# Kernel tuning notes

Hardware: AMD Instinct MI355X
Metric: run time of the kernel (lower is better)

Reference implementation:

```python
import jax, jax.numpy as jnp
import numpy as np
import math

N, E, O, C, KD, KEYD = 50000, 800000, 4, 64, 16, 128


def setup_inputs() -> dict:
    key = jax.random.key(0)
    ks = jax.random.split(key, 10)
    x = jax.random.normal(ks[0], (N, O, C), jnp.float32)
    kernel_basis = jax.random.normal(ks[1], (E, O, KD), jnp.float32)
    fiber_kernel_basis = jax.random.normal(ks[2], (O, O, KD), jnp.float32)
    edge_index = jax.random.randint(ks[3], (2, E), 0, N, jnp.int32)
    # nn.Linear default init ~ U(-1/sqrt(fan_in), 1/sqrt(fan_in)); scaled normal is fine as data
    kernel_W = jax.random.normal(ks[4], (C, KD), jnp.float32) / math.sqrt(KD)        # kernel: Linear(kernel_dim -> in_channels)
    fiber_kernel_W = jax.random.normal(ks[5], (C, KD), jnp.float32) / math.sqrt(KD)  # depthwise: in*out/groups = C
    key_W = jax.random.normal(ks[6], (KEYD, C), jnp.float32) / math.sqrt(C)
    key_b = jnp.zeros((KEYD,), jnp.float32)
    query_W = jax.random.normal(ks[7], (KEYD, C), jnp.float32) / math.sqrt(C)
    query_b = jnp.zeros((KEYD,), jnp.float32)
    bias = jnp.zeros((C,), jnp.float32)
    return {"x": x, "kernel_basis": kernel_basis, "fiber_kernel_basis": fiber_kernel_basis,
            "edge_index": edge_index, "kernel_W": kernel_W, "fiber_kernel_W": fiber_kernel_W,
            "key_W": key_W, "key_b": key_b, "query_W": query_W, "query_b": query_b, "bias": bias}


def reference(x, kernel_basis, fiber_kernel_basis, edge_index, kernel_W, fiber_kernel_W,
              key_W, key_b, query_W, query_b, bias):
    src = edge_index[0]
    dst = edge_index[1]
    n = x.shape[0]
    # per-edge spatial kernel: [E,O,KD] @ [KD,C] -> [E,O,C]
    k = jnp.einsum('eok,ck->eoc', kernel_basis, kernel_W)
    message = x[src] * k                                       # [E,O,C]
    # scatter-softmax attention over incoming edges of each target node
    keys = jnp.einsum('noc,kc->nok', x, key_W) + key_b        # [N,O,KEYD]
    queries = jnp.einsum('noc,kc->nok', x, query_W) + query_b
    logits = jnp.sum(keys[src] * queries[dst], axis=-1, keepdims=True) / math.sqrt(KEYD)  # [E,O,1]
    e = jnp.exp(logits - jnp.max(logits))                      # global-max stabilization, as in source
    denom = jax.ops.segment_sum(e, dst, num_segments=n) + 1e-6 # [N,O,1]
    att = e / denom[dst]
    message = message * att
    # scatter-add aggregation into target nodes
    x1 = jax.ops.segment_sum(message, dst, num_segments=n)     # [N,O,C]
    # fiber (orientation) mixing kernel: [O,O,KD] @ [KD,C] -> [O,O,C]
    fk = jnp.einsum('pok,ck->poc', fiber_kernel_basis, fiber_kernel_W)
    x2 = jnp.einsum('boc,poc->bpc', x1, fk) / fk.shape[-2]
    return x2 + bias
```

## Files before the change

### kernel.cpp

```cpp
#include <hip/hip_runtime.h>
#include <math.h>

#define NN 50000
#define EE 800000
#define OO 4
#define CC 64
#define KDD 16
#define KEYDD 128
#define CH 16

typedef float v2f __attribute__((ext_vector_type(2)));

__device__ __forceinline__ float wave_red_sum(float v) {
  int x;
  x = __builtin_amdgcn_update_dpp(0, __float_as_int(v), 0x111, 0xf, 0xf, false);
  v += __int_as_float(x);
  x = __builtin_amdgcn_update_dpp(0, __float_as_int(v), 0x112, 0xf, 0xf, false);
  v += __int_as_float(x);
  x = __builtin_amdgcn_update_dpp(0, __float_as_int(v), 0x114, 0xf, 0xf, false);
  v += __int_as_float(x);
  x = __builtin_amdgcn_update_dpp(0, __float_as_int(v), 0x118, 0xf, 0xf, false);
  v += __int_as_float(x);
  x = __builtin_amdgcn_update_dpp(0, __float_as_int(v), 0x142, 0xa, 0xf, false);
  v += __int_as_float(x);
  x = __builtin_amdgcn_update_dpp(0, __float_as_int(v), 0x143, 0xc, 0xf, false);
  v += __int_as_float(x);
  return __int_as_float(__builtin_amdgcn_readlane(__float_as_int(v), 63));
}

__device__ __forceinline__ float exp2_fast(float x) {
  float r;
  asm("v_exp_f32 %0, %1" : "=v"(r) : "v"(x));
  return r;
}

__device__ __forceinline__ void red4(float q0, float q1, float q2, float q3,
                                     float& p0, float& p1, float& p2, float& p3) {
  asm("s_nop 1\n\tv_permlane32_swap_b32 %0, %1" : "+v"(q0), "+v"(q1));
  float ra = q0 + q1;
  asm("s_nop 1\n\tv_permlane32_swap_b32 %0, %1" : "+v"(q2), "+v"(q3));
  float rb = q2 + q3;
  asm("s_nop 1\n\t"
      "v_add_f32_dpp %0, %0, %0 row_shr:1 row_mask:0xf bank_mask:0xf bound_ctrl:0\n\t"
      "v_add_f32_dpp %1, %1, %1 row_shr:1 row_mask:0xf bank_mask:0xf bound_ctrl:0\n\t"
      "v_add_f32_dpp %0, %0, %0 row_shr:2 row_mask:0xf bank_mask:0xf bound_ctrl:0\n\t"
      "v_add_f32_dpp %1, %1, %1 row_shr:2 row_mask:0xf bank_mask:0xf bound_ctrl:0\n\t"
      "v_add_f32_dpp %0, %0, %0 row_shr:4 row_mask:0xf bank_mask:0xf bound_ctrl:0\n\t"
      "v_add_f32_dpp %1, %1, %1 row_shr:4 row_mask:0xf bank_mask:0xf bound_ctrl:0\n\t"
      "v_add_f32_dpp %0, %0, %0 row_shr:8 row_mask:0xf bank_mask:0xf bound_ctrl:0\n\t"
      "v_add_f32_dpp %1, %1, %1 row_shr:8 row_mask:0xf bank_mask:0xf bound_ctrl:0\n\t"
      "v_add_f32_dpp %0, %0, %0 row_bcast:15 row_mask:0xa bank_mask:0xf bound_ctrl:0\n\t"
      "v_add_f32_dpp %1, %1, %1 row_bcast:15 row_mask:0xa bank_mask:0xf bound_ctrl:0\n\t"
      "s_nop 0"
      : "+v"(ra), "+v"(rb));
  p0 = __int_as_float(__builtin_amdgcn_readlane(__float_as_int(ra), 31));
  p1 = __int_as_float(__builtin_amdgcn_readlane(__float_as_int(ra), 63));
  p2 = __int_as_float(__builtin_amdgcn_readlane(__float_as_int(rb), 31));
  p3 = __int_as_float(__builtin_amdgcn_readlane(__float_as_int(rb), 63));
}

__global__ void prep_kernel(const float* __restrict__ keyW, const float* __restrict__ keyB,
                            const float* __restrict__ qryW, const float* __restrict__ qryB,
                            const float* __restrict__ fkb, const float* __restrict__ fkw,
                            float* __restrict__ Mt, float* __restrict__ aVec,
                            float* __restrict__ bVec, float* __restrict__ c0,
                            float* __restrict__ fk) {
  __shared__ float qw[KEYDD * CC];
  __shared__ float kws[KEYDD * 4];
  int t = threadIdx.x, b = blockIdx.x;
  if (b < 16) {
    for (int i = t; i < KEYDD * CC; i += 256) qw[i] = qryW[i];
    for (int i = t; i < KEYDD * 4; i += 256) {
      int k = i >> 2, c1l = i & 3;
      kws[i] = keyW[k * CC + b * 4 + c1l];
    }
    __syncthreads();
    int c1l = t >> 6, c2 = t & 63;
    float s = 0.f;
    #pragma unroll 8
    for (int k = 0; k < KEYDD; ++k)
      s = fmaf(kws[k * 4 + c1l], qw[k * CC + c2], s);
    Mt[c2 * CC + b * 4 + c1l] = s;
  } else {
    if (t < CC) {
      float sa = 0.f, sb = 0.f;
      for (int k = 0; k < KEYDD; ++k) {
        sa = fmaf(keyB[k], qryW[k * CC + t], sa);
        sb = fmaf(qryB[k], keyW[k * CC + t], sb);
      }
      aVec[t] = sa; bVec[t] = sb;
    }
    if (t == 0) {
      float s = 0.f;
      for (int k = 0; k < KEYDD; ++k) s = fmaf(keyB[k], qryB[k], s);
      c0[0] = s;
    }
    for (int idx = t; idx < OO * OO * CC; idx += 256) {
      int p = idx >> 8, rem = idx & 255;
      int o = rem >> 6, c = rem & 63;
      float s = 0.f;
      #pragma unroll
      for (int kd = 0; kd < KDD; ++kd)
        s = fmaf(fkb[(p * OO + o) * KDD + kd], fkw[c * KDD + kd], s);
      fk[idx] = 0.25f * s;
    }
  }
}

__global__ void count_kernel(const int* __restrict__ ei, int* __restrict__ counts) {
  int e = blockIdx.x * 256 + threadIdx.x;
  if (e < EE) atomicAdd(&counts[ei[EE + e]], 1);
}

__global__ void scan1_kernel(const int* __restrict__ counts, int* __restrict__ incl,
                             int* __restrict__ bsum, int n) {
  __shared__ int buf[256];
  int t = threadIdx.x;
  int i = blockIdx.x * 256 + t;
  int v = (i < n) ? counts[i] : 0;
  buf[t] = v;
  __syncthreads();
  for (int off = 1; off < 256; off <<= 1) {
    int a = buf[t];
    int b2 = (t >= off) ? buf[t - off] : 0;
    __syncthreads();
    buf[t] = a + b2;
    __syncthreads();
  }
  if (i < n) incl[i] = buf[t];
  if (t == 255) bsum[blockIdx.x] = buf[255];
}
__global__ void scan2_kernel(const int* __restrict__ bsum, int* __restrict__ bbase, int nb) {
  __shared__ int buf[256];
  int t = threadIdx.x;
  int v = (t < nb) ? bsum[t] : 0;
  buf[t] = v;
  __syncthreads();
  for (int off = 1; off < 256; off <<= 1) {
    int a = buf[t];
    int b2 = (t >= off) ? buf[t - off] : 0;
    __syncthreads();
    buf[t] = a + b2;
    __syncthreads();
  }
  if (t < nb) bbase[t] = buf[t] - v;
}
__global__ void scan3_kernel(const int* __restrict__ counts, const int* __restrict__ incl,
                             const int* __restrict__ bbase, int* __restrict__ offsets, int n) {
  int i = blockIdx.x * 256 + threadIdx.x;
  if (i < n) {
    int oi = bbase[blockIdx.x] + incl[i];
    offsets[i] = oi - counts[i];
    if (i == n - 1) offsets[n] = oi;
  }
}

__global__ void fill_kernel(const int* __restrict__ ei, const int* __restrict__ offsets,
                            int* __restrict__ counts, long long* __restrict__ pairs) {
  int e = blockIdx.x * 256 + threadIdx.x;
  if (e < EE) {
    int d = ei[EE + e];
    int r = atomicSub(&counts[d], 1) - 1;
    int pos = offsets[d] + r;
    pairs[pos] = ((long long)ei[e] << 32) | (unsigned)e;
  }
}

__device__ __forceinline__ float kv_dot(const float* __restrict__ kb, int ej, int obase,
                                        float4 kw0, float4 kw1, float4 kw2, float4 kw3) {
  const float4* bp = reinterpret_cast<const float4*>(kb + ej * (OO * KDD) + obase);
  float4 b0 = bp[0], b1 = bp[1], b2 = bp[2], b3 = bp[3];
  v2f a0 = {0.f, 0.f}, a1 = {0.f, 0.f};
  #define P2(f4, i) (reinterpret_cast<const v2f*>(&(f4))[i])
  a0 = __builtin_elementwise_fma(P2(b0, 0), P2(kw0, 0), a0);
  a1 = __builtin_elementwise_fma(P2(b0, 1), P2(kw0, 1), a1);
  a0 = __builtin_elementwise_fma(P2(b1, 0), P2(kw1, 0), a0);
  a1 = __builtin_elementwise_fma(P2(b1, 1), P2(kw1, 1), a1);
  a0 = __builtin_elementwise_fma(P2(b2, 0), P2(kw2, 0), a0);
  a1 = __builtin_elementwise_fma(P2(b2, 1), P2(kw2, 1), a1);
  a0 = __builtin_elementwise_fma(P2(b3, 0), P2(kw3, 0), a0);
  a1 = __builtin_elementwise_fma(P2(b3, 1), P2(kw3, 1), a1);
  #undef P2
  v2f s = a0 + a1;
  return s.x + s.y;
}

__global__ __launch_bounds__(256, 4) void mega_kernel(
    const float* __restrict__ x, const float* __restrict__ Mt,
    const float* __restrict__ aVec, const float* __restrict__ bVec,
    const float* __restrict__ c0p, const float* __restrict__ kb,
    const float* __restrict__ kW, const int* __restrict__ offsets,
    const long long* __restrict__ pairs, const float* __restrict__ fkg,
    const float* __restrict__ bias, float* __restrict__ out) {
  __shared__ float x1[OO * CC];
  int n = blockIdx.x;
  int t = threadIdx.x;
  int o = __builtin_amdgcn_readfirstlane(t >> 6);
  int c = t & 63;
  const float scale2 = 0.12751541050862828f;
  int js = offsets[n], je = offsets[n + 1];
  int deg = je - js;

  int lane16 = c & 15;
  long long pr = 0;
  if (deg > 0) pr = pairs[js + min(lane16, deg - 1)];

  int rowoff = __builtin_amdgcn_readfirstlane((n * OO + o) * CC);
  const float* xrow = x + rowoff;
  float ub0 = 0.f, ub1 = 0.f, ub2 = 0.f, ub3 = 0.f;
  #pragma unroll
  for (int q = 0; q < 16; ++q) {
    ub0 = fmaf(Mt[(4 * q + 0) * CC + c], xrow[4 * q + 0], ub0);
    ub1 = fmaf(Mt[(4 * q + 1) * CC + c], xrow[4 * q + 1], ub1);
    ub2 = fmaf(Mt[(4 * q + 2) * CC + c], xrow[4 * q + 2], ub2);
    ub3 = fmaf(Mt[(4 * q + 3) * CC + c], xrow[4 * q + 3], ub3);
  }
  float ubr = (((ub0 + ub1) + (ub2 + ub3)) + bVec[c]) * scale2;
  float xown = xrow[c];
  float base2 = (wave_red_sum(aVec[c] * xown) + c0p[0]) * scale2;

  const float4* kwp = reinterpret_cast<const float4*>(kW + c * KDD);
  float4 kw0 = kwp[0], kw1 = kwp[1], kw2 = kwp[2], kw3 = kwp[3];
  int obase = o * KDD;
  int voff = c << 2;

  float S = 0.f, acc = 0.f;

  for (int cs = 0; cs < deg; cs += CH) {
    int cl = deg - cs; if (cl > CH) cl = CH;
    int e_v = (int)((unsigned long long)pr & 0xffffffffu);
    int s_v = (int)(pr >> 32);
    float xv[CH];
    #pragma unroll
    for (int j = 0; j < CH; ++j) {
      int sj = __builtin_amdgcn_readlane(s_v, j);
      const float* pj = x + (size_t)(sj * OO + o) * CC;
      asm volatile("global_load_dword %0, %1, %2"
                   : "=v"(xv[j]) : "v"(voff), "s"(pj));
    }
    asm volatile("s_waitcnt vmcnt(0)" ::: "memory");
    __builtin_amdgcn_sched_barrier(0);
    int ns = cs + CH;
    if (ns < deg) {
      int ncl = deg - ns;
      pr = pairs[js + ns + min(lane16, ncl - 1)];
    }
    __builtin_amdgcn_sched_barrier(0);
    #define SUB4(J0)                                                           \
    {                                                                          \
      float kv0 = kv_dot(kb, __builtin_amdgcn_readlane(e_v, (J0) + 0), obase, kw0, kw1, kw2, kw3); \
      float kv1 = kv_dot(kb, __builtin_amdgcn_readlane(e_v, (J0) + 1), obase, kw0, kw1, kw2, kw3); \
      float kv2 = kv_dot(kb, __builtin_amdgcn_readlane(e_v, (J0) + 2), obase, kw0, kw1, kw2, kw3); \
      float kv3 = kv_dot(kb, __builtin_amdgcn_readlane(e_v, (J0) + 3), obase, kw0, kw1, kw2, kw3); \
      float p0, p1, p2, p3;                                                    \
      red4(xv[(J0) + 0] * ubr, xv[(J0) + 1] * ubr,                             \
           xv[(J0) + 2] * ubr, xv[(J0) + 3] * ubr, p0, p1, p2, p3);            \
      float ev0 = ((J0) + 0 < cl) ? exp2_fast(p0) : 0.f;                       \
      float ev1 = ((J0) + 1 < cl) ? exp2_fast(p1) : 0.f;                       \
      float ev2 = ((J0) + 2 < cl) ? exp2_fast(p2) : 0.f;                       \
      float ev3 = ((J0) + 3 < cl) ? exp2_fast(p3) : 0.f;                       \
      S += (ev0 + ev1) + (ev2 + ev3);                                          \
      acc = fmaf(ev0 * kv0, xv[(J0) + 0], acc);                                \
      acc = fmaf(ev1 * kv1, xv[(J0) + 1], acc);                                \
      acc = fmaf(ev2 * kv2, xv[(J0) + 2], acc);                                \
      acc = fmaf(ev3 * kv3, xv[(J0) + 3], acc);                                \
    }
    SUB4(0)
    if (cl > 4)  SUB4(4)
    if (cl > 8)  SUB4(8)
    if (cl > 12) SUB4(12)
    #undef SUB4
  }

  float invd = 1.0f / (S + 1e-6f * exp2_fast(-base2));
  x1[t] = acc * invd;
  __syncthreads();
  float s2s = 0.f;
  #pragma unroll
  for (int oo = 0; oo < OO; ++oo)
    s2s = fmaf(x1[oo * CC + c], fkg[o * (OO * CC) + oo * CC + c], s2s);
  out[(size_t)n * (OO * CC) + t] = s2s + bias[c];
}

extern "C" void kernel_launch(void* const* d_in, const int* in_sizes, int n_in,
                              void* d_out, int out_size, void* d_ws, size_t ws_size,
                              hipStream_t stream) {
  const float* x    = (const float*)d_in[0];
  const float* kb   = (const float*)d_in[1];
  const float* fkb  = (const float*)d_in[2];
  const int*   ei   = (const int*)d_in[3];
  const float* kW   = (const float*)d_in[4];
  const float* fkW  = (const float*)d_in[5];
  const float* keyW = (const float*)d_in[6];
  const float* keyB = (const float*)d_in[7];
  const float* qryW = (const float*)d_in[8];
  const float* qryB = (const float*)d_in[9];
  const float* bias = (const float*)d_in[10];
  float* out = (float*)d_out;

  const int NB = (NN + 255) / 256;

  float* wsf  = (float*)d_ws;
  float* Mt   = wsf;
  float* aVec = Mt + 4096;
  float* bVec = aVec + 64;
  float* c0   = bVec + 64;
  float* fk   = c0 + 64;
  long long* pairs = (long long*)(fk + 1024);
  int* counts    = (int*)(pairs + EE);
  int* offsets   = counts + NN;
  int* incl      = offsets + NN + 1;
  int* bsum      = incl + NN;
  int* bbase     = bsum + 256;

  hipMemsetAsync(counts, 0, (size_t)NN * sizeof(int), stream);

  prep_kernel<<<17, 256, 0, stream>>>(keyW, keyB, qryW, qryB, fkb, fkW, Mt, aVec, bVec, c0, fk);
  count_kernel<<<(EE + 255) / 256, 256, 0, stream>>>(ei, counts);
  scan1_kernel<<<NB, 256, 0, stream>>>(counts, incl, bsum, NN);
  scan2_kernel<<<1, 256, 0, stream>>>(bsum, bbase, NB);
  scan3_kernel<<<NB, 256, 0, stream>>>(counts, incl, bbase, offsets, NN);
  fill_kernel<<<(EE + 255) / 256, 256, 0, stream>>>(ei, offsets, counts, pairs);
  mega_kernel<<<NN, 256, 0, stream>>>(x, Mt, aVec, bVec, c0, kb, kW, offsets, pairs,
                                      fk, bias, out);
}
```

Baseline: 407.5 us.

## Double-buffer neighbor gathers and split edge pairs into separate index arrays

The mega kernel's edge loop now uses two register buffers, so the x gathers for the next 16-edge chunk and the index loads for the chunk after are issued before the current chunk is computed. This hides gather latency behind the kernel-basis dot products and exp work. The packed 64-bit (src, edge) pairs are split into two int arrays that are loaded with inline asm. The cost is extra VGPRs for a second 16-float buffer and the edge-id arrays, which may lower occupancy under the 256x4 launch bounds. Nodes average 16 edges, so many have only one chunk and get little overlap.

```diff
diff --git a/kernel.cpp b/kernel.cpp
--- a/kernel.cpp
+++ b/kernel.cpp
@@ -156,13 +156,15 @@
 }
 
 __global__ void fill_kernel(const int* __restrict__ ei, const int* __restrict__ offsets,
-                            int* __restrict__ counts, long long* __restrict__ pairs) {
+                            int* __restrict__ counts, int* __restrict__ edge_list,
+                            int* __restrict__ esrc) {
   int e = blockIdx.x * 256 + threadIdx.x;
   if (e < EE) {
     int d = ei[EE + e];
     int r = atomicSub(&counts[d], 1) - 1;
     int pos = offsets[d] + r;
-    pairs[pos] = ((long long)ei[e] << 32) | (unsigned)e;
+    edge_list[pos] = e;
+    esrc[pos] = ei[e];
   }
 }
 
@@ -190,8 +192,9 @@
     const float* __restrict__ aVec, const float* __restrict__ bVec,
     const float* __restrict__ c0p, const float* __restrict__ kb,
     const float* __restrict__ kW, const int* __restrict__ offsets,
-    const long long* __restrict__ pairs, const float* __restrict__ fkg,
-    const float* __restrict__ bias, float* __restrict__ out) {
+    const int* __restrict__ edge_list, const int* __restrict__ esrc,
+    const float* __restrict__ fkg, const float* __restrict__ bias,
+    float* __restrict__ out) {
   __shared__ float x1[OO * CC];
   int n = blockIdx.x;
   int t = threadIdx.x;
@@ -200,10 +203,14 @@
   const float scale2 = 0.12751541050862828f;
   int js = offsets[n], je = offsets[n + 1];
   int deg = je - js;
-
   int lane16 = c & 15;
-  long long pr = 0;
-  if (deg > 0) pr = pairs[js + min(lane16, deg - 1)];
+
+  int eA = 0, sA = 0, eB = 0, sB = 0;
+  if (deg > 0) {
+    int q0 = (js + min(lane16, deg - 1)) << 2;
+    asm volatile("global_load_dword %0, %1, %2" : "=v"(eA) : "v"(q0), "s"(edge_list));
+    asm volatile("global_load_dword %0, %1, %2" : "=v"(sA) : "v"(q0), "s"(esrc));
+  }
 
   int rowoff = __builtin_amdgcn_readfirstlane((n * OO + o) * CC);
   const float* xrow = x + rowoff;
@@ -225,52 +232,102 @@
   int voff = c << 2;
 
   float S = 0.f, acc = 0.f;
-
-  for (int cs = 0; cs < deg; cs += CH) {
-    int cl = deg - cs; if (cl > CH) cl = CH;
-    int e_v = (int)((unsigned long long)pr & 0xffffffffu);
-    int s_v = (int)(pr >> 32);
-    float xv[CH];
-    #pragma unroll
-    for (int j = 0; j < CH; ++j) {
-      int sj = __builtin_amdgcn_readlane(s_v, j);
-      const float* pj = x + (size_t)(sj * OO + o) * CC;
-      asm volatile("global_load_dword %0, %1, %2"
-                   : "=v"(xv[j]) : "v"(voff), "s"(pj));
-    }
+  float xvA[CH], xvB[CH];
+
+  #define GATHER(XV, SV)                                                       \
+  {                                                                            \
+    _Pragma("unroll")                                                          \
+    for (int j = 0; j < CH; ++j) {                                             \
+      int sj = __builtin_amdgcn_readlane(SV, j);                               \
+      const float* pj = x + (size_t)(sj * OO + o) * CC;                        \
+      asm volatile("global_load_dword %0, %1, %2"                              \
+                   : "=v"(XV[j]) : "v"(voff), "s"(pj));                        \
+    }                                                                          \
+  }
+  #define SUB4(XV, ES, J0, CL)                                                 \
+  {                                                                            \
+    float kv0 = kv_dot(kb, ES[(J0) + 0], obase, kw0, kw1, kw2, kw3);           \
+    float kv1 = kv_dot(kb, ES[(J0) + 1], obase, kw0, kw1, kw2, kw3);           \
+    float kv2 = kv_dot(kb, ES[(J0) + 2], obase, kw0, kw1, kw2, kw3);           \
+    float kv3 = kv_dot(kb, ES[(J0) + 3], obase, kw0, kw1, kw2, kw3);           \
+    float p0, p1, p2, p3;                                                      \
+    red4(XV[(J0) + 0] * ubr, XV[(J0) + 1] * ubr,                               \
+         XV[(J0) + 2] * ubr, XV[(J0) + 3] * ubr, p0, p1, p2, p3);              \
+    float ev0 = ((J0) + 0 < (CL)) ? exp2_fast(p0) : 0.f;                       \
+    float ev1 = ((J0) + 1 < (CL)) ? exp2_fast(p1) : 0.f;                       \
+    float ev2 = ((J0) + 2 < (CL)) ? exp2_fast(p2) : 0.f;                       \
+    float ev3 = ((J0) + 3 < (CL)) ? exp2_fast(p3) : 0.f;                       \
+    S += (ev0 + ev1) + (ev2 + ev3);                                            \
+    acc = fmaf(ev0 * kv0, XV[(J0) + 0], acc);                                  \
+    acc = fmaf(ev1 * kv1, XV[(J0) + 1], acc);                                  \
+    acc = fmaf(ev2 * kv2, XV[(J0) + 2], acc);                                  \
+    acc = fmaf(ev3 * kv3, XV[(J0) + 3], acc);                                  \
+  }
+  #define COMPUTE(XV, ES, CL)                                                  \
+    SUB4(XV, ES, 0, CL)                                                        \
+    if ((CL) > 4)  SUB4(XV, ES, 4, CL)                                         \
+    if ((CL) > 8)  SUB4(XV, ES, 8, CL)                                         \
+    if ((CL) > 12) SUB4(XV, ES, 12, CL)
+
+  if (deg > 0) {
     asm volatile("s_waitcnt vmcnt(0)" ::: "memory");
     __builtin_amdgcn_sched_barrier(0);
-    int ns = cs + CH;
-    if (ns < deg) {
-      int ncl = deg - ns;
-      pr = pairs[js + ns + min(lane16, ncl - 1)];
-    }
-    __builtin_amdgcn_sched_barrier(0);
-    #define SUB4(J0)                                                           \
-    {                                                                          \
-      float kv0 = kv_dot(kb, __builtin_amdgcn_readlane(e_v, (J0) + 0), obase, kw0, kw1, kw2, kw3); \
-      float kv1 = kv_dot(kb, __builtin_amdgcn_readlane(e_v, (J0) + 1), obase, kw0, kw1, kw2, kw3); \
-      float kv2 = kv_dot(kb, __builtin_amdgcn_readlane(e_v, (J0) + 2), obase, kw0, kw1, kw2, kw3); \
-      float kv3 = kv_dot(kb, __builtin_amdgcn_readlane(e_v, (J0) + 3), obase, kw0, kw1, kw2, kw3); \
-      float p0, p1, p2, p3;                                                    \
-      red4(xv[(J0) + 0] * ubr, xv[(J0) + 1] * ubr,                             \
-           xv[(J0) + 2] * ubr, xv[(J0) + 3] * ubr, p0, p1, p2, p3);            \
-      float ev0 = ((J0) + 0 < cl) ? exp2_fast(p0) : 0.f;                       \
-      float ev1 = ((J0) + 1 < cl) ? exp2_fast(p1) : 0.f;                       \
-      float ev2 = ((J0) + 2 < cl) ? exp2_fast(p2) : 0.f;                       \
-      float ev3 = ((J0) + 3 < cl) ? exp2_fast(p3) : 0.f;                       \
-      S += (ev0 + ev1) + (ev2 + ev3);                                          \
-      acc = fmaf(ev0 * kv0, xv[(J0) + 0], acc);                                \
-      acc = fmaf(ev1 * kv1, xv[(J0) + 1], acc);                                \
-      acc = fmaf(ev2 * kv2, xv[(J0) + 2], acc);                                \
-      acc = fmaf(ev3 * kv3, xv[(J0) + 3], acc);                                \
-    }
-    SUB4(0)
-    if (cl > 4)  SUB4(4)
-    if (cl > 8)  SUB4(8)
-    if (cl > 12) SUB4(12)
-    #undef SUB4
-  }
+    GATHER(xvA, sA)
+    if (CH < deg) {
+      int rem = deg - CH;
+      int q1 = (js + CH + min(lane16, rem - 1)) << 2;
+      asm volatile("global_load_dword %0, %1, %2" : "=v"(eB) : "v"(q1), "s"(edge_list));
+      asm volatile("global_load_dword %0, %1, %2" : "=v"(sB) : "v"(q1), "s"(esrc));
+    }
+    int cs = 0;
+    while (true) {
+      asm volatile("s_waitcnt vmcnt(0)" ::: "memory");
+      __builtin_amdgcn_sched_barrier(0);
+      int cl = deg - cs; if (cl > CH) cl = CH;
+      int esA[CH];
+      #pragma unroll
+      for (int j = 0; j < CH; ++j) esA[j] = __builtin_amdgcn_readlane(eA, j);
+      bool hasNext = (cs + CH) < deg;
+      if (hasNext) {
+        GATHER(xvB, sB)
+        int ns2 = cs + 2 * CH;
+        if (ns2 < deg) {
+          int rem2 = deg - ns2;
+          int q2 = (js + ns2 + min(lane16, rem2 - 1)) << 2;
+          asm volatile("global_load_dword %0, %1, %2" : "=v"(eA) : "v"(q2), "s"(edge_list));
+          asm volatile("global_load_dword %0, %1, %2" : "=v"(sA) : "v"(q2), "s"(esrc));
+        }
+      }
+      __builtin_amdgcn_sched_barrier(0);
+      COMPUTE(xvA, esA, cl)
+      if (!hasNext) break;
+      cs += CH;
+      asm volatile("s_waitcnt vmcnt(0)" ::: "memory");
+      __builtin_amdgcn_sched_barrier(0);
+      cl = deg - cs; if (cl > CH) cl = CH;
+      int esB[CH];
+      #pragma unroll
+      for (int j = 0; j < CH; ++j) esB[j] = __builtin_amdgcn_readlane(eB, j);
+      hasNext = (cs + CH) < deg;
+      if (hasNext) {
+        GATHER(xvA, sA)
+        int ns2 = cs + 2 * CH;
+        if (ns2 < deg) {
+          int rem2 = deg - ns2;
+          int q2 = (js + ns2 + min(lane16, rem2 - 1)) << 2;
+          asm volatile("global_load_dword %0, %1, %2" : "=v"(eB) : "v"(q2), "s"(edge_list));
+          asm volatile("global_load_dword %0, %1, %2" : "=v"(sB) : "v"(q2), "s"(esrc));
+        }
+      }
+      __builtin_amdgcn_sched_barrier(0);
+      COMPUTE(xvB, esB, cl)
+      if (!hasNext) break;
+      cs += CH;
+    }
+  }
+  #undef COMPUTE
+  #undef SUB4
+  #undef GATHER
 
   float invd = 1.0f / (S + 1e-6f * exp2_fast(-base2));
   x1[t] = acc * invd;
@@ -306,8 +363,9 @@
   float* bVec = aVec + 64;
   float* c0   = bVec + 64;
   float* fk   = c0 + 64;
-  long long* pairs = (long long*)(fk + 1024);
-  int* counts    = (int*)(pairs + EE);
+  int* edge_list = (int*)(fk + 1024);
+  int* esrc      = edge_list + EE;
+  int* counts    = esrc + EE;
   int* offsets   = counts + NN;
   int* incl      = offsets + NN + 1;
   int* bsum      = incl + NN;
@@ -320,7 +378,7 @@
   scan1_kernel<<<NB, 256, 0, stream>>>(counts, incl, bsum, NN);
   scan2_kernel<<<1, 256, 0, stream>>>(bsum, bbase, NB);
   scan3_kernel<<<NB, 256, 0, stream>>>(counts, incl, bbase, offsets, NN);
-  fill_kernel<<<(EE + 255) / 256, 256, 0, stream>>>(ei, offsets, counts, pairs);
-  mega_kernel<<<NN, 256, 0, stream>>>(x, Mt, aVec, bVec, c0, kb, kW, offsets, pairs,
-                                      fk, bias, out);
-}
+  fill_kernel<<<(EE + 255) / 256, 256, 0, stream>>>(ei, offsets, counts, edge_list, esrc);
+  mega_kernel<<<NN, 256, 0, stream>>>(x, Mt, aVec, bVec, c0, kb, kW, offsets,
+                                      edge_list, esrc, fk, bias, out);
+}
```

After: 1.581 ms. 3.88x slower.

## Double-buffer per-edge kernel basis rows in LDS via async global-to-LDS loads

Applied to the files above, without the earlier changes.

Per-edge kernel_basis rows for each 16-edge chunk are now staged cooperatively into a double-buffered LDS array with global_load_lds, and the pair indices are prefetched two chunks ahead. Each wave fetches its share of the 256-byte rows, and the dot products read from LDS instead of issuing scalar-addressed global float4 loads per edge. The aim is to overlap the next chunk's basis fetch with the current chunk's compute and to avoid redundant global reads across the four orientation waves. The cost is a block-wide __syncthreads per chunk and extra LDS use, which may lower occupancy.

```diff
diff --git a/kernel.cpp b/kernel.cpp
--- a/kernel.cpp
+++ b/kernel.cpp
@@ -59,6 +59,12 @@
   p3 = __int_as_float(__builtin_amdgcn_readlane(__float_as_int(rb), 63));
 }
 
+__device__ __forceinline__ void async_cp16(const float* gsrc, float* ldst) {
+  __builtin_amdgcn_global_load_lds(
+      (const __attribute__((address_space(1))) unsigned int*)gsrc,
+      (__attribute__((address_space(3))) unsigned int*)ldst, 16, 0, 0);
+}
+
 __global__ void prep_kernel(const float* __restrict__ keyW, const float* __restrict__ keyB,
                             const float* __restrict__ qryW, const float* __restrict__ qryB,
                             const float* __restrict__ fkb, const float* __restrict__ fkw,
@@ -166,9 +172,9 @@
   }
 }
 
-__device__ __forceinline__ float kv_dot(const float* __restrict__ kb, int ej, int obase,
-                                        float4 kw0, float4 kw1, float4 kw2, float4 kw3) {
-  const float4* bp = reinterpret_cast<const float4*>(kb + ej * (OO * KDD) + obase);
+__device__ __forceinline__ float kv_dot_lds(const float* row,
+                                            float4 kw0, float4 kw1, float4 kw2, float4 kw3) {
+  const float4* bp = reinterpret_cast<const float4*>(row);
   float4 b0 = bp[0], b1 = bp[1], b2 = bp[2], b3 = bp[3];
   v2f a0 = {0.f, 0.f}, a1 = {0.f, 0.f};
   #define P2(f4, i) (reinterpret_cast<const v2f*>(&(f4))[i])
@@ -192,6 +198,7 @@
     const float* __restrict__ kW, const int* __restrict__ offsets,
     const long long* __restrict__ pairs, const float* __restrict__ fkg,
     const float* __restrict__ bias, float* __restrict__ out) {
+  __shared__ float kbL[2][CH * 64];
   __shared__ float x1[OO * CC];
   int n = blockIdx.x;
   int t = threadIdx.x;
@@ -200,10 +207,10 @@
   const float scale2 = 0.12751541050862828f;
   int js = offsets[n], je = offsets[n + 1];
   int deg = je - js;
-
   int lane16 = c & 15;
-  long long pr = 0;
-  if (deg > 0) pr = pairs[js + min(lane16, deg - 1)];
+
+  long long prA = 0;
+  if (deg > 0) prA = pairs[js + min(lane16, deg - 1)];
 
   int rowoff = __builtin_amdgcn_readfirstlane((n * OO + o) * CC);
   const float* xrow = x + rowoff;
@@ -223,13 +230,34 @@
   float4 kw0 = kwp[0], kw1 = kwp[1], kw2 = kwp[2], kw3 = kwp[3];
   int obase = o * KDD;
   int voff = c << 2;
+  int w4 = o * 4;
+  int ksel = c >> 4;
+
+  #define STAGE(BUF, EV)                                                       \
+  {                                                                            \
+    int e0 = __builtin_amdgcn_readlane(EV, w4 + 0);                            \
+    int e1 = __builtin_amdgcn_readlane(EV, w4 + 1);                            \
+    int e2 = __builtin_amdgcn_readlane(EV, w4 + 2);                            \
+    int e3 = __builtin_amdgcn_readlane(EV, w4 + 3);                            \
+    int elo = (ksel & 1) ? e1 : e0;                                            \
+    int ehi = (ksel & 1) ? e3 : e2;                                            \
+    int es = (ksel & 2) ? ehi : elo;                                           \
+    async_cp16(kb + (size_t)es * 64 + (c & 15) * 4, &kbL[BUF][w4 * 64]);       \
+  }
 
   float S = 0.f, acc = 0.f;
+
+  if (deg > 0) {
+    int eA0 = (int)((unsigned long long)prA & 0xffffffffu);
+    STAGE(0, eA0)
+  }
+  long long prB = 0;
+  if (CH < deg) prB = pairs[js + CH + min(lane16, deg - CH - 1)];
 
   for (int cs = 0; cs < deg; cs += CH) {
     int cl = deg - cs; if (cl > CH) cl = CH;
-    int e_v = (int)((unsigned long long)pr & 0xffffffffu);
-    int s_v = (int)(pr >> 32);
+    int buf = (cs >> 4) & 1;
+    int s_v = (int)(prA >> 32);
     float xv[CH];
     #pragma unroll
     for (int j = 0; j < CH; ++j) {
@@ -240,18 +268,22 @@
     }
     asm volatile("s_waitcnt vmcnt(0)" ::: "memory");
     __builtin_amdgcn_sched_barrier(0);
-    int ns = cs + CH;
-    if (ns < deg) {
-      int ncl = deg - ns;
-      pr = pairs[js + ns + min(lane16, ncl - 1)];
-    }
+    __syncthreads();
+    bool hasNext = (cs + CH) < deg;
+    if (hasNext) {
+      int eN = (int)((unsigned long long)prB & 0xffffffffu);
+      STAGE(buf ^ 1, eN)
+    }
+    prA = prB;
+    int ns2 = cs + 2 * CH;
+    if (ns2 < deg) prB = pairs[js + ns2 + min(lane16, deg - ns2 - 1)];
     __builtin_amdgcn_sched_barrier(0);
     #define SUB4(J0)                                                           \
     {                                                                          \
-      float kv0 = kv_dot(kb, __builtin_amdgcn_readlane(e_v, (J0) + 0), obase, kw0, kw1, kw2, kw3); \
-      float kv1 = kv_dot(kb, __builtin_amdgcn_readlane(e_v, (J0) + 1), obase, kw0, kw1, kw2, kw3); \
-      float kv2 = kv_dot(kb, __builtin_amdgcn_readlane(e_v, (J0) + 2), obase, kw0, kw1, kw2, kw3); \
-      float kv3 = kv_dot(kb, __builtin_amdgcn_readlane(e_v, (J0) + 3), obase, kw0, kw1, kw2, kw3); \
+      float kv0 = kv_dot_lds(&kbL[buf][((J0) + 0) * 64 + obase], kw0, kw1, kw2, kw3); \
+      float kv1 = kv_dot_lds(&kbL[buf][((J0) + 1) * 64 + obase], kw0, kw1, kw2, kw3); \
+      float kv2 = kv_dot_lds(&kbL[buf][((J0) + 2) * 64 + obase], kw0, kw1, kw2, kw3); \
+      float kv3 = kv_dot_lds(&kbL[buf][((J0) + 3) * 64 + obase], kw0, kw1, kw2, kw3); \
       float p0, p1, p2, p3;                                                    \
       red4(xv[(J0) + 0] * ubr, xv[(J0) + 1] * ubr,                             \
            xv[(J0) + 2] * ubr, xv[(J0) + 3] * ubr, p0, p1, p2, p3);            \
@@ -271,6 +303,7 @@
     if (cl > 12) SUB4(12)
     #undef SUB4
   }
+  #undef STAGE
 
   float invd = 1.0f / (S + 1e-6f * exp2_fast(-base2));
   x1[t] = acc * invd;
```

Measured after the change: 436.4 us. +7.1%, slower.

## Double-buffer neighbor gathers with all edge pairs preloaded per wave

Applied to the files above, without the earlier changes.

Loads up to 64 (edge, src) pairs per node once into lanes instead of reloading 16 per chunk. The gather loop becomes a ping-pong double buffer of 8-element chunks, so the next chunk's x-row loads are issued before the current chunk is computed. This hides gather latency behind the dot-product and exp work. Nodes with degree above 64 fall back to a serial per-edge tail loop, which is slow but rare for average degree 16. The extra register buffer may raise register pressure.

```diff
diff --git a/kernel.cpp b/kernel.cpp
--- a/kernel.cpp
+++ b/kernel.cpp
@@ -7,7 +7,7 @@
 #define CC 64
 #define KDD 16
 #define KEYDD 128
-#define CH 16
+#define CH 8
 
 typedef float v2f __attribute__((ext_vector_type(2)));
 
@@ -200,10 +200,10 @@
   const float scale2 = 0.12751541050862828f;
   int js = offsets[n], je = offsets[n + 1];
   int deg = je - js;
-
-  int lane16 = c & 15;
-  long long pr = 0;
-  if (deg > 0) pr = pairs[js + min(lane16, deg - 1)];
+  int dm1 = deg - 1;
+
+  long long prAll = 0;
+  if (deg > 0) prAll = pairs[js + min(c, dm1)];
 
   int rowoff = __builtin_amdgcn_readfirstlane((n * OO + o) * CC);
   const float* xrow = x + rowoff;
@@ -224,52 +224,89 @@
   int obase = o * KDD;
   int voff = c << 2;
 
+  int e_all = (int)((unsigned long long)prAll & 0xffffffffu);
+  int s_all = (int)(prAll >> 32);
+
   float S = 0.f, acc = 0.f;
-
-  for (int cs = 0; cs < deg; cs += CH) {
-    int cl = deg - cs; if (cl > CH) cl = CH;
-    int e_v = (int)((unsigned long long)pr & 0xffffffffu);
-    int s_v = (int)(pr >> 32);
-    float xv[CH];
-    #pragma unroll
-    for (int j = 0; j < CH; ++j) {
-      int sj = __builtin_amdgcn_readlane(s_v, j);
-      const float* pj = x + (size_t)(sj * OO + o) * CC;
-      asm volatile("global_load_dword %0, %1, %2"
-                   : "=v"(xv[j]) : "v"(voff), "s"(pj));
-    }
-    asm volatile("s_waitcnt vmcnt(0)" ::: "memory");
-    __builtin_amdgcn_sched_barrier(0);
-    int ns = cs + CH;
-    if (ns < deg) {
-      int ncl = deg - ns;
-      pr = pairs[js + ns + min(lane16, ncl - 1)];
-    }
-    __builtin_amdgcn_sched_barrier(0);
-    #define SUB4(J0)                                                           \
-    {                                                                          \
-      float kv0 = kv_dot(kb, __builtin_amdgcn_readlane(e_v, (J0) + 0), obase, kw0, kw1, kw2, kw3); \
-      float kv1 = kv_dot(kb, __builtin_amdgcn_readlane(e_v, (J0) + 1), obase, kw0, kw1, kw2, kw3); \
-      float kv2 = kv_dot(kb, __builtin_amdgcn_readlane(e_v, (J0) + 2), obase, kw0, kw1, kw2, kw3); \
-      float kv3 = kv_dot(kb, __builtin_amdgcn_readlane(e_v, (J0) + 3), obase, kw0, kw1, kw2, kw3); \
-      float p0, p1, p2, p3;                                                    \
-      red4(xv[(J0) + 0] * ubr, xv[(J0) + 1] * ubr,                             \
-           xv[(J0) + 2] * ubr, xv[(J0) + 3] * ubr, p0, p1, p2, p3);            \
-      float ev0 = ((J0) + 0 < cl) ? exp2_fast(p0) : 0.f;                       \
-      float ev1 = ((J0) + 1 < cl) ? exp2_fast(p1) : 0.f;                       \
-      float ev2 = ((J0) + 2 < cl) ? exp2_fast(p2) : 0.f;                       \
-      float ev3 = ((J0) + 3 < cl) ? exp2_fast(p3) : 0.f;                       \
-      S += (ev0 + ev1) + (ev2 + ev3);                                          \
-      acc = fmaf(ev0 * kv0, xv[(J0) + 0], acc);                                \
-      acc = fmaf(ev1 * kv1, xv[(J0) + 1], acc);                                \
-      acc = fmaf(ev2 * kv2, xv[(J0) + 2], acc);                                \
-      acc = fmaf(ev3 * kv3, xv[(J0) + 3], acc);                                \
-    }
-    SUB4(0)
-    if (cl > 4)  SUB4(4)
-    if (cl > 8)  SUB4(8)
-    if (cl > 12) SUB4(12)
-    #undef SUB4
+  int degc = min(deg, 64);
+
+  #define GATHER(XV, CS)                                                       \
+  {                                                                            \
+    _Pragma("unroll")                                                          \
+    for (int j = 0; j < CH; ++j) {                                             \
+      int li = (CS) + j; li = (li < dm1) ? li : dm1;                           \
+      int sj = __builtin_amdgcn_readlane(s_all, li);                           \
+      const float* pj = x + (size_t)(sj * OO + o) * CC;                        \
+      asm volatile("global_load_dword %0, %1, %2"                              \
+                   : "=v"(XV[j]) : "v"(voff), "s"(pj));                        \
+    }                                                                          \
+  }
+  #define SUB4(XV, CS, J0, CL)                                                 \
+  {                                                                            \
+    int la = (CS)+(J0)+0; la = (la < dm1) ? la : dm1;                          \
+    int lb = (CS)+(J0)+1; lb = (lb < dm1) ? lb : dm1;                          \
+    int lc2 = (CS)+(J0)+2; lc2 = (lc2 < dm1) ? lc2 : dm1;                      \
+    int ld = (CS)+(J0)+3; ld = (ld < dm1) ? ld : dm1;                          \
+    float kv0 = kv_dot(kb, __builtin_amdgcn_readlane(e_all, la), obase, kw0, kw1, kw2, kw3);  \
+    float kv1 = kv_dot(kb, __builtin_amdgcn_readlane(e_all, lb), obase, kw0, kw1, kw2, kw3);  \
+    float kv2 = kv_dot(kb, __builtin_amdgcn_readlane(e_all, lc2), obase, kw0, kw1, kw2, kw3); \
+    float kv3 = kv_dot(kb, __builtin_amdgcn_readlane(e_all, ld), obase, kw0, kw1, kw2, kw3);  \
+    float p0, p1, p2, p3;                                                      \
+    red4(XV[(J0) + 0] * ubr, XV[(J0) + 1] * ubr,                               \
+         XV[(J0) + 2] * ubr, XV[(J0) + 3] * ubr, p0, p1, p2, p3);              \
+    float ev0 = ((J0) + 0 < (CL)) ? exp2_fast(p0) : 0.f;                       \
+    float ev1 = ((J0) + 1 < (CL)) ? exp2_fast(p1) : 0.f;                       \
+    float ev2 = ((J0) + 2 < (CL)) ? exp2_fast(p2) : 0.f;                       \
+    float ev3 = ((J0) + 3 < (CL)) ? exp2_fast(p3) : 0.f;                       \
+    S += (ev0 + ev1) + (ev2 + ev3);                                            \
+    acc = fmaf(ev0 * kv0, XV[(J0) + 0], acc);                                  \
+    acc = fmaf(ev1 * kv1, XV[(J0) + 1], acc);                                  \
+    acc = fmaf(ev2 * kv2, XV[(J0) + 2], acc);                                  \
+    acc = fmaf(ev3 * kv3, XV[(J0) + 3], acc);                                  \
+  }
+  #define COMPUTE(XV, CS, CL)                                                  \
+    SUB4(XV, CS, 0, CL)                                                        \
+    if ((CL) > 4) SUB4(XV, CS, 4, CL)
+
+  if (degc > 0) {
+    float xvA[CH], xvB[CH];
+    GATHER(xvA, 0)
+    int cs = 0;
+    while (true) {
+      int cl = degc - cs; if (cl > CH) cl = CH;
+      bool hasNext = (cs + CH) < degc;
+      asm volatile("s_waitcnt vmcnt(0)" ::: "memory");
+      __builtin_amdgcn_sched_barrier(0);
+      if (hasNext) GATHER(xvB, cs + CH)
+      __builtin_amdgcn_sched_barrier(0);
+      COMPUTE(xvA, cs, cl)
+      if (!hasNext) break;
+      cs += CH;
+      cl = degc - cs; if (cl > CH) cl = CH;
+      hasNext = (cs + CH) < degc;
+      asm volatile("s_waitcnt vmcnt(0)" ::: "memory");
+      __builtin_amdgcn_sched_barrier(0);
+      if (hasNext) GATHER(xvA, cs + CH)
+      __builtin_amdgcn_sched_barrier(0);
+      COMPUTE(xvB, cs, cl)
+      if (!hasNext) break;
+      cs += CH;
+    }
+  }
+  #undef COMPUTE
+  #undef SUB4
+  #undef GATHER
+
+  for (int eidx = 64; eidx < deg; ++eidx) {
+    long long pp = pairs[js + eidx];
+    int sid = __builtin_amdgcn_readfirstlane((int)(pp >> 32));
+    int eid = __builtin_amdgcn_readfirstlane((int)((unsigned long long)pp & 0xffffffffu));
+    float xe = x[(size_t)(sid * OO + o) * CC + c];
+    float p = wave_red_sum(xe * ubr);
+    float ev = exp2_fast(p);
+    float kv = kv_dot(kb, eid, obase, kw0, kw1, kw2, kw3);
+    S += ev;
+    acc = fmaf(ev * kv, xe, acc);
   }
 
   float invd = 1.0f / (S + 1e-6f * exp2_fast(-base2));
```

Result: no change. 404.3 us (-0.8%).
